# Performance work log

Measured on AMD Instinct MI355X. Metric: run time of the kernel, lower is better.

The kernel has to match this reference:

```python
import jax, jax.numpy as jnp
import numpy as np

BN_EPS = 1e-5

def setup_inputs() -> dict:
    key = jax.random.key(0)
    ks = jax.random.split(key, 5)
    B, C, H, W = 4, 64, 64, 64
    s = 1.0 / np.sqrt(C)
    return {
        "x": jax.random.normal(ks[0], (B, C, H, W), dtype=jnp.float32),
        "Wk": jax.random.normal(ks[1], (C, C), dtype=jnp.float32) * s,
        "Wq": jax.random.normal(ks[2], (C, C), dtype=jnp.float32) * s,
        "Wv": jax.random.normal(ks[3], (C, C), dtype=jnp.float32) * s,
        "W2": jax.random.normal(ks[4], (C, C), dtype=jnp.float32) * s,
        "gamma": jnp.ones((C,), dtype=jnp.float32),
        "beta": jnp.zeros((C,), dtype=jnp.float32),
        "running_mean": jnp.zeros((C,), dtype=jnp.float32),
        "running_var": jnp.ones((C,), dtype=jnp.float32),
    }

def reference(x, Wk, Wq, Wv, W2, gamma, beta, running_mean, running_var):
    B, C, H, W = x.shape
    N = H * W
    xf = x.reshape(B, C, N)                      # flatten spatial -> (B,C,N)
    # 1x1 convs (no bias) == channel matmuls
    k = jnp.einsum('oc,bcn->bon', Wk, xf)        # (B,C,N)
    q = jnp.einsum('oc,bcn->bon', Wq, xf)
    v = jnp.einsum('oc,bcn->bon', Wv, xf)
    # scores[b,n,m] = sum_c k[b,c,n] * q[b,c,m]  (note: no 1/sqrt(d) scaling, as in source)
    scores = jnp.einsum('bcn,bcm->bnm', k, q)    # (B,N,N)
    p = jax.nn.softmax(scores, axis=2)
    # att[b,c,n] = sum_m p[b,n,m] * v[b,c,m]
    att = jnp.einsum('bnm,bcm->bcn', p, v)       # (B,C,N)
    y = jnp.einsum('oc,bcn->bon', W2, att)       # 1x1 conv
    inv = gamma / jnp.sqrt(running_var + BN_EPS)
    y = y * inv[None, :, None] + (beta - running_mean * inv)[None, :, None]
    y = jax.nn.relu(y)
    return y.reshape(B, C, H, W) + x
```

## Files before the change

### kernel.cpp

```cpp
#include <hip/hip_runtime.h>

#define CH   64
#define NTOT 4096
#define NB   4
#define L2E  1.44269504088896340736f

typedef short  short4v  __attribute__((ext_vector_type(4)));
typedef short  short8v  __attribute__((ext_vector_type(8)));
typedef float  floatx4  __attribute__((ext_vector_type(4)));

static __device__ __forceinline__ unsigned pk2bf(float lo, float hi) {
    unsigned r;
    asm("v_cvt_pk_bf16_f32 %0, %1, %2" : "=v"(r) : "v"(lo), "v"(hi));
    return r;
}
static __device__ __forceinline__ float ex2(float x) {
    return __builtin_amdgcn_exp2f(x);
}
static __device__ __forceinline__ short f2bf(float f) {
    union { float f; unsigned u; } v; v.f = f;
    unsigned r = v.u + 0x7FFFu + ((v.u >> 16) & 1u);
    return (short)(r >> 16);
}
static __device__ __forceinline__ float bf2f(short s) {
    union { unsigned u; float f; } v; v.u = ((unsigned)(unsigned short)s) << 16;
    return v.f;
}

__global__ __launch_bounds__(256) void qkv_mfma(
    const float* __restrict__ x,
    const float* __restrict__ Wk, const float* __restrict__ Wq,
    const float* __restrict__ Wv,
    short* __restrict__ kT, short* __restrict__ qT, short* __restrict__ vg)
{
    __shared__ __align__(16) short xhi[64 * 72];
    __shared__ __align__(16) short xlo[64 * 72];
    __shared__ __align__(16) short whi[64 * 72];
    __shared__ __align__(16) short wlo[64 * 72];

    const int tid = threadIdx.x;
    const int w = tid >> 6, l = tid & 63, g = l >> 4, ln = l & 15;
    const int b  = blockIdx.x >> 6;
    const int n0 = (blockIdx.x & 63) << 6;
    const float* xb = x + ((size_t)b << 18);

    #pragma unroll
    for (int i = 0; i < 4; ++i) {
        int idx = tid + (i << 8);
        int c = idx >> 4, n4 = (idx & 15) << 2;
        float4 xv = *(const float4*)&xb[c * 4096 + n0 + n4];
        float xa[4] = {xv.x, xv.y, xv.z, xv.w};
        #pragma unroll
        for (int j = 0; j < 4; ++j) {
            short h = f2bf(xa[j]);
            xhi[(n4 + j) * 72 + c] = h;
            xlo[(n4 + j) * 72 + c] = f2bf(xa[j] - bf2f(h));
        }
    }

    const int wo = tid >> 2, wc = (tid & 3) << 4;
    #pragma unroll
    for (int j2 = 0; j2 < 4; ++j2) {
        float4 a = *(const float4*)&Wk[wo * 64 + wc + (j2 << 2)];
        float aa[4] = {a.x, a.y, a.z, a.w};
        #pragma unroll
        for (int j = 0; j < 4; ++j) {
            short h = f2bf(aa[j]);
            whi[wo * 72 + wc + (j2 << 2) + j] = h;
            wlo[wo * 72 + wc + (j2 << 2) + j] = f2bf(aa[j] - bf2f(h));
        }
    }
    __syncthreads();

    short8v xh0 = *(const short8v*)&xhi[((w << 4) + ln) * 72 + (g << 3)];
    short8v xh1 = *(const short8v*)&xhi[((w << 4) + ln) * 72 + 32 + (g << 3)];
    short8v xl0 = *(const short8v*)&xlo[((w << 4) + ln) * 72 + (g << 3)];
    short8v xl1 = *(const short8v*)&xlo[((w << 4) + ln) * 72 + 32 + (g << 3)];

    #pragma unroll
    for (int m = 0; m < 3; ++m) {
        if (m > 0) {
            const float* W = (m == 1) ? Wq : Wv;
            #pragma unroll
            for (int j2 = 0; j2 < 4; ++j2) {
                float4 a = *(const float4*)&W[wo * 64 + wc + (j2 << 2)];
                float aa[4] = {a.x, a.y, a.z, a.w};
                #pragma unroll
                for (int j = 0; j < 4; ++j) {
                    short h = f2bf(aa[j]);
                    whi[wo * 72 + wc + (j2 << 2) + j] = h;
                    wlo[wo * 72 + wc + (j2 << 2) + j] = f2bf(aa[j] - bf2f(h));
                }
            }
            __syncthreads();
        }

        #pragma unroll
        for (int ot = 0; ot < 4; ++ot) {
            short8v ah0 = *(const short8v*)&whi[((ot << 4) + ln) * 72 + (g << 3)];
            short8v ah1 = *(const short8v*)&whi[((ot << 4) + ln) * 72 + 32 + (g << 3)];
            short8v al0 = *(const short8v*)&wlo[((ot << 4) + ln) * 72 + (g << 3)];
            short8v al1 = *(const short8v*)&wlo[((ot << 4) + ln) * 72 + 32 + (g << 3)];
            floatx4 acc = (floatx4){0.f, 0.f, 0.f, 0.f};
            if (m < 2) {
                acc = __builtin_amdgcn_mfma_f32_16x16x32_bf16(ah0, xh0, acc, 0, 0, 0);
                acc = __builtin_amdgcn_mfma_f32_16x16x32_bf16(ah1, xh1, acc, 0, 0, 0);
                acc = __builtin_amdgcn_mfma_f32_16x16x32_bf16(al0, xh0, acc, 0, 0, 0);
                acc = __builtin_amdgcn_mfma_f32_16x16x32_bf16(al1, xh1, acc, 0, 0, 0);
                acc = __builtin_amdgcn_mfma_f32_16x16x32_bf16(ah0, xl0, acc, 0, 0, 0);
                acc = __builtin_amdgcn_mfma_f32_16x16x32_bf16(ah1, xl1, acc, 0, 0, 0);
                short* dst = ((m == 0) ? kT : qT) + ((size_t)b << 18);
                uint2 p;
                p.x = pk2bf(acc[0], acc[1]);
                p.y = pk2bf(acc[2], acc[3]);
                *(uint2*)&dst[(size_t)(n0 + (w << 4) + ln) * 64 + (ot << 4) + (g << 2)] = p;
            } else {
                acc = __builtin_amdgcn_mfma_f32_16x16x32_bf16(xh0, ah0, acc, 0, 0, 0);
                acc = __builtin_amdgcn_mfma_f32_16x16x32_bf16(xh1, ah1, acc, 0, 0, 0);
                acc = __builtin_amdgcn_mfma_f32_16x16x32_bf16(xl0, ah0, acc, 0, 0, 0);
                acc = __builtin_amdgcn_mfma_f32_16x16x32_bf16(xl1, ah1, acc, 0, 0, 0);
                acc = __builtin_amdgcn_mfma_f32_16x16x32_bf16(xh0, al0, acc, 0, 0, 0);
                acc = __builtin_amdgcn_mfma_f32_16x16x32_bf16(xh1, al1, acc, 0, 0, 0);
                short* dst = vg + ((size_t)b << 18);
                uint2 p;
                p.x = pk2bf(acc[0], acc[1]);
                p.y = pk2bf(acc[2], acc[3]);
                *(uint2*)&dst[(size_t)((ot << 4) + ln) * 4096 + n0 + (w << 4) + (g << 2)] = p;
            }
        }
        __syncthreads();
    }
}

__global__ __launch_bounds__(256) void attn_partial(
    const short* __restrict__ kT, const short* __restrict__ qT,
    const short* __restrict__ vg,
    float* __restrict__ opart, float* __restrict__ mlpart)
{
    __shared__ __align__(16) short smem[27648];

    const int tid = threadIdx.x;
    const int w = tid >> 6, l = tid & 63, g = l >> 4, ln = l & 15;

    const int bid = blockIdx.x;
    const int xcd = bid & 7, grp = bid >> 3;
    const int bk  = (xcd << 1) | (grp >> 5);
    const int b   = bk >> 2, kc = bk & 3;
    const int qblk = grp & 31;
    const int n0   = qblk << 7;
    const int part = (((b << 2) | kc) << 5) | qblk;
    const int kbase = kc << 10;

    const short* kTb = kT + ((size_t)b << 18) + (size_t)n0 * 64;
    const short* qTb = qT + ((size_t)b << 18);
    const short* vb  = vg + ((size_t)b << 18);

    short* const kTs = smem;
    short* const qS  = smem + 9216;
    short* const vS  = smem + 13824;
    short* const PsW = smem + 18432 + w * 2304;

    #pragma unroll
    for (int j = 0; j < 4; ++j) {
        int row = tid >> 1, c8 = ((tid & 1) << 5) + (j << 3);
        *(short8v*)&kTs[row * 72 + c8] = *(const short8v*)&kTb[row * 64 + c8];
    }
    __syncthreads();

    short8v bS0 = *(const short8v*)&kTs[((w << 5) + ln) * 72 + (g << 3)];
    short8v bS1 = *(const short8v*)&kTs[((w << 5) + ln) * 72 + 32 + (g << 3)];
    short8v bS2 = *(const short8v*)&kTs[((w << 5) + 16 + ln) * 72 + (g << 3)];
    short8v bS3 = *(const short8v*)&kTs[((w << 5) + 16 + ln) * 72 + 32 + (g << 3)];

    float mrun0 = -1e30f, lrun0 = 0.f;
    float mrun1 = -1e30f, lrun1 = 0.f;
    floatx4 acc0[4], acc1[4];
    #pragma unroll
    for (int ct = 0; ct < 4; ++ct) {
        acc0[ct] = (floatx4){0.f, 0.f, 0.f, 0.f};
        acc1[ct] = (floatx4){0.f, 0.f, 0.f, 0.f};
    }

    const int i0 = tid, i1 = tid + 256;

    short8v pf[4];
    pf[0] = *(const short8v*)&qTb[(size_t)(kbase + (i0 >> 3)) * 64 + ((i0 & 7) << 3)];
    pf[1] = *(const short8v*)&qTb[(size_t)(kbase + (i1 >> 3)) * 64 + ((i1 & 7) << 3)];
    pf[2] = *(const short8v*)&vb[(size_t)(i0 >> 3) * 4096 + kbase + ((i0 & 7) << 3)];
    pf[3] = *(const short8v*)&vb[(size_t)(i1 >> 3) * 4096 + kbase + ((i1 & 7) << 3)];

    for (int t = 0; t < 16; ++t) {
        __syncthreads();
        *(short8v*)&qS[(i0 >> 3) * 72 + ((i0 & 7) << 3)] = pf[0];
        *(short8v*)&qS[(i1 >> 3) * 72 + ((i1 & 7) << 3)] = pf[1];
        *(short8v*)&vS[(i0 >> 3) * 72 + ((i0 & 7) << 3)] = pf[2];
        *(short8v*)&vS[(i1 >> 3) * 72 + ((i1 & 7) << 3)] = pf[3];
        __syncthreads();
        if (t < 15) {
            int m1 = kbase + ((t + 1) << 6);
            pf[0] = *(const short8v*)&qTb[(size_t)(m1 + (i0 >> 3)) * 64 + ((i0 & 7) << 3)];
            pf[1] = *(const short8v*)&qTb[(size_t)(m1 + (i1 >> 3)) * 64 + ((i1 & 7) << 3)];
            pf[2] = *(const short8v*)&vb[(size_t)(i0 >> 3) * 4096 + m1 + ((i0 & 7) << 3)];
            pf[3] = *(const short8v*)&vb[(size_t)(i1 >> 3) * 4096 + m1 + ((i1 & 7) << 3)];
        }

        floatx4 s0[4], s1[4];
        #pragma unroll
        for (int mt = 0; mt < 4; ++mt) {
            short8v a0 = *(const short8v*)&qS[((mt << 4) + ln) * 72 + (g << 3)];
            short8v a1 = *(const short8v*)&qS[((mt << 4) + ln) * 72 + 32 + (g << 3)];
            floatx4 acc = (floatx4){0.f, 0.f, 0.f, 0.f};
            acc = __builtin_amdgcn_mfma_f32_16x16x32_bf16(a0, bS0, acc, 0, 0, 0);
            acc = __builtin_amdgcn_mfma_f32_16x16x32_bf16(a1, bS1, acc, 0, 0, 0);
            s0[mt] = acc;
            acc = (floatx4){0.f, 0.f, 0.f, 0.f};
            acc = __builtin_amdgcn_mfma_f32_16x16x32_bf16(a0, bS2, acc, 0, 0, 0);
            acc = __builtin_amdgcn_mfma_f32_16x16x32_bf16(a1, bS3, acc, 0, 0, 0);
            s1[mt] = acc;
        }

        {
            float mx = s0[0][0];
            #pragma unroll
            for (int mt = 0; mt < 4; ++mt)
                #pragma unroll
                for (int r = 0; r < 4; ++r) mx = fmaxf(mx, s0[mt][r]);
            mx = fmaxf(mx, __shfl_xor(mx, 16));
            mx = fmaxf(mx, __shfl_xor(mx, 32));
            if (!__all(mx <= mrun0)) {
                float mnew = fmaxf(mrun0, mx);
                float fs = ex2((mrun0 - mnew) * L2E);
                mrun0 = mnew;
                lrun0 *= fs;
                #pragma unroll
                for (int ct = 0; ct < 4; ++ct) {
                    acc0[ct][0] *= fs; acc0[ct][1] *= fs;
                    acc0[ct][2] *= fs; acc0[ct][3] *= fs;
                }
            }
            const float nm = -mrun0 * L2E;
            float s = 0.f;
            #pragma unroll
            for (int mt = 0; mt < 4; ++mt) {
                float p0 = ex2(__builtin_fmaf(s0[mt][0], L2E, nm));
                float p1 = ex2(__builtin_fmaf(s0[mt][1], L2E, nm));
                float p2 = ex2(__builtin_fmaf(s0[mt][2], L2E, nm));
                float p3 = ex2(__builtin_fmaf(s0[mt][3], L2E, nm));
                s += (p0 + p1) + (p2 + p3);
                uint2 pkv;
                pkv.x = pk2bf(p0, p1);
                pkv.y = pk2bf(p2, p3);
                *(uint2*)&PsW[ln * 72 + (mt << 4) + (g << 2)] = pkv;
            }
            s += __shfl_xor(s, 16);
            s += __shfl_xor(s, 32);
            lrun0 += s;
        }
        {
            float mx = s1[0][0];
            #pragma unroll
            for (int mt = 0; mt < 4; ++mt)
                #pragma unroll
                for (int r = 0; r < 4; ++r) mx = fmaxf(mx, s1[mt][r]);
            mx = fmaxf(mx, __shfl_xor(mx, 16));
            mx = fmaxf(mx, __shfl_xor(mx, 32));
            if (!__all(mx <= mrun1)) {
                float mnew = fmaxf(mrun1, mx);
                float fs = ex2((mrun1 - mnew) * L2E);
                mrun1 = mnew;
                lrun1 *= fs;
                #pragma unroll
                for (int ct = 0; ct < 4; ++ct) {
                    acc1[ct][0] *= fs; acc1[ct][1] *= fs;
                    acc1[ct][2] *= fs; acc1[ct][3] *= fs;
                }
            }
            const float nm = -mrun1 * L2E;
            float s = 0.f;
            #pragma unroll
            for (int mt = 0; mt < 4; ++mt) {
                float p0 = ex2(__builtin_fmaf(s1[mt][0], L2E, nm));
                float p1 = ex2(__builtin_fmaf(s1[mt][1], L2E, nm));
                float p2 = ex2(__builtin_fmaf(s1[mt][2], L2E, nm));
                float p3 = ex2(__builtin_fmaf(s1[mt][3], L2E, nm));
                s += (p0 + p1) + (p2 + p3);
                uint2 pkv;
                pkv.x = pk2bf(p0, p1);
                pkv.y = pk2bf(p2, p3);
                *(uint2*)&PsW[(16 + ln) * 72 + (mt << 4) + (g << 2)] = pkv;
            }
            s += __shfl_xor(s, 16);
            s += __shfl_xor(s, 32);
            lrun1 += s;
        }

        short8v bp0 = *(const short8v*)&PsW[ln * 72 + (g << 3)];
        short8v bp1 = *(const short8v*)&PsW[ln * 72 + 32 + (g << 3)];
        short8v bp2 = *(const short8v*)&PsW[(16 + ln) * 72 + (g << 3)];
        short8v bp3 = *(const short8v*)&PsW[(16 + ln) * 72 + 32 + (g << 3)];
        #pragma unroll
        for (int ct = 0; ct < 4; ++ct) {
            short8v a0 = *(const short8v*)&vS[((ct << 4) + ln) * 72 + (g << 3)];
            short8v a1 = *(const short8v*)&vS[((ct << 4) + ln) * 72 + 32 + (g << 3)];
            acc0[ct] = __builtin_amdgcn_mfma_f32_16x16x32_bf16(a0, bp0, acc0[ct], 0, 0, 0);
            acc0[ct] = __builtin_amdgcn_mfma_f32_16x16x32_bf16(a1, bp1, acc0[ct], 0, 0, 0);
            acc1[ct] = __builtin_amdgcn_mfma_f32_16x16x32_bf16(a0, bp2, acc1[ct], 0, 0, 0);
            acc1[ct] = __builtin_amdgcn_mfma_f32_16x16x32_bf16(a1, bp3, acc1[ct], 0, 0, 0);
        }
    }

    __syncthreads();
    float* xp = (float*)(smem + 9216);
    #pragma unroll
    for (int ct = 0; ct < 4; ++ct)
        #pragma unroll
        for (int r = 0; r < 4; ++r) {
            xp[((w << 5) + ln) * 68 + (ct << 4) + (g << 2) + r]      = acc0[ct][r];
            xp[((w << 5) + 16 + ln) * 68 + (ct << 4) + (g << 2) + r] = acc1[ct][r];
        }
    if (g == 0) {
        mlpart[(size_t)part * 256 + (w << 5) + ln]            = mrun0;
        mlpart[(size_t)part * 256 + (w << 5) + 16 + ln]       = mrun1;
        mlpart[(size_t)part * 256 + 128 + (w << 5) + ln]      = lrun0;
        mlpart[(size_t)part * 256 + 128 + (w << 5) + 16 + ln] = lrun1;
    }
    __syncthreads();
    {
        int q = tid >> 1, c32 = (tid & 1) << 5;
        float* Ob = opart + (size_t)part * 8192 + q * 64 + c32;
        const float* Xp = &xp[q * 68 + c32];
        #pragma unroll
        for (int j = 0; j < 8; ++j)
            *(float4*)&Ob[j << 2] = *(const float4*)&Xp[j << 2];
    }
}

__global__ __launch_bounds__(256) void attn_merge(
    const float* __restrict__ opart, const float* __restrict__ mlpart,
    const float* __restrict__ W2,
    const float* __restrict__ gamma, const float* __restrict__ beta,
    const float* __restrict__ rmean, const float* __restrict__ rvar,
    const float* __restrict__ x, float* __restrict__ out)
{
    __shared__ __align__(16) short attL[64 * 72];
    __shared__ __align__(16) short w2s [64 * 72];
    __shared__ float wgt[4][64];
    __shared__ float linv[64];

    const int tid = threadIdx.x;
    const int w = tid >> 6, l = tid & 63, g = l >> 4, ln = l & 15;

    const int b      = blockIdx.x >> 6;
    const int qblk64 = blockIdx.x & 63;
    const int n0     = qblk64 << 6;
    const int qb128  = qblk64 >> 1;
    const int qoff   = (qblk64 & 1) << 6;

    if (tid < 64) {
        float mv[4], lv[4];
        #pragma unroll
        for (int kc = 0; kc < 4; ++kc) {
            int part = (((b << 2) | kc) << 5) | qb128;
            mv[kc] = mlpart[(size_t)part * 256 + qoff + tid];
            lv[kc] = mlpart[(size_t)part * 256 + 128 + qoff + tid];
        }
        float mm = fmaxf(fmaxf(mv[0], mv[1]), fmaxf(mv[2], mv[3]));
        float den = 0.f;
        #pragma unroll
        for (int kc = 0; kc < 4; ++kc) {
            float wk = ex2((mv[kc] - mm) * L2E);
            wgt[kc][tid] = wk;
            den += wk * lv[kc];
        }
        linv[tid] = 1.0f / den;
    }
    for (int i = tid; i < 1024; i += 256) {
        int r = i >> 4, c4 = (i & 15) << 2;
        float4 wv = *(const float4*)&W2[(r << 6) + c4];
        uint2 s4;
        s4.x = pk2bf(wv.x, wv.y);
        s4.y = pk2bf(wv.z, wv.w);
        *(uint2*)&w2s[r * 72 + c4] = s4;
    }
    __syncthreads();

    {
        int q = tid >> 2, c16 = (tid & 3) << 4;
        float a[16] = {};
        #pragma unroll
        for (int kc = 0; kc < 4; ++kc) {
            int part = (((b << 2) | kc) << 5) | qb128;
            float wk = wgt[kc][q];
            const float* Ob = opart + (size_t)part * 8192 + (qoff + q) * 64 + c16;
            #pragma unroll
            for (int i = 0; i < 4; ++i) {
                float4 o4 = *(const float4*)&Ob[i << 2];
                a[(i << 2) + 0] += wk * o4.x;
                a[(i << 2) + 1] += wk * o4.y;
                a[(i << 2) + 2] += wk * o4.z;
                a[(i << 2) + 3] += wk * o4.w;
            }
        }
        float li = linv[q];
        #pragma unroll
        for (int i = 0; i < 4; ++i) {
            uint2 s4;
            s4.x = pk2bf(a[(i << 2) + 0] * li, a[(i << 2) + 1] * li);
            s4.y = pk2bf(a[(i << 2) + 2] * li, a[(i << 2) + 3] * li);
            *(uint2*)&attL[q * 72 + c16 + (i << 2)] = s4;
        }
    }
    __syncthreads();

    short8v bA0 = *(const short8v*)&attL[((w << 4) + ln) * 72 + (g << 3)];
    short8v bA1 = *(const short8v*)&attL[((w << 4) + ln) * 72 + 32 + (g << 3)];
    const int nq = n0 + (w << 4) + ln;
    #pragma unroll
    for (int ot = 0; ot < 4; ++ot) {
        short8v a0 = *(const short8v*)&w2s[((ot << 4) + ln) * 72 + (g << 3)];
        short8v a1 = *(const short8v*)&w2s[((ot << 4) + ln) * 72 + 32 + (g << 3)];
        floatx4 acc = (floatx4){0.f, 0.f, 0.f, 0.f};
        acc = __builtin_amdgcn_mfma_f32_16x16x32_bf16(a0, bA0, acc, 0, 0, 0);
        acc = __builtin_amdgcn_mfma_f32_16x16x32_bf16(a1, bA1, acc, 0, 0, 0);
        int o0 = (ot << 4) + (g << 2);
        float4 gm = *(const float4*)&gamma[o0];
        float4 bt = *(const float4*)&beta [o0];
        float4 rm = *(const float4*)&rmean[o0];
        float4 rv = *(const float4*)&rvar [o0];
        float gma[4] = {gm.x, gm.y, gm.z, gm.w};
        float bta[4] = {bt.x, bt.y, bt.z, bt.w};
        float rma[4] = {rm.x, rm.y, rm.z, rm.w};
        float rva[4] = {rv.x, rv.y, rv.z, rv.w};
        #pragma unroll
        for (int r = 0; r < 4; ++r) {
            float inv  = gma[r] * __frsqrt_rn(rva[r] + 1e-5f);
            float bias = bta[r] - rma[r] * inv;
            size_t ga = (((size_t)(b << 6) + o0 + r) << 12) + nq;
            out[ga] = fmaxf(acc[r] * inv + bias, 0.f) + x[ga];
        }
    }
}

extern "C" void kernel_launch(void* const* d_in, const int* in_sizes, int n_in,
                              void* d_out, int out_size, void* d_ws, size_t ws_size,
                              hipStream_t stream)
{
    const float* x     = (const float*)d_in[0];
    const float* Wk    = (const float*)d_in[1];
    const float* Wq    = (const float*)d_in[2];
    const float* Wv    = (const float*)d_in[3];
    const float* W2    = (const float*)d_in[4];
    const float* gamma = (const float*)d_in[5];
    const float* beta  = (const float*)d_in[6];
    const float* rmean = (const float*)d_in[7];
    const float* rvar  = (const float*)d_in[8];
    float* out = (float*)d_out;

    const size_t plane = (size_t)NB * NTOT * CH;
    short* kT = (short*)d_ws;
    short* qT = kT + plane;
    short* vv = qT + plane;
    float* opart  = (float*)(vv + plane);
    float* mlpart = opart + (size_t)512 * 8192;

    qkv_mfma    <<<dim3(256), dim3(256), 0, stream>>>(x, Wk, Wq, Wv, kT, qT, vv);
    attn_partial<<<dim3(512), dim3(256), 0, stream>>>(kT, qT, vv, opart, mlpart);
    attn_merge  <<<dim3(256), dim3(256), 0, stream>>>(opart, mlpart, W2, gamma, beta,
                                                      rmean, rvar, x, out);
}
```

Before: 62.88 us.

## Load attention Q/V fragments straight from global, drop LDS staging and block barriers

The attention partial kernel no longer stages K, Q and V tiles through shared memory with block-wide barriers. Each wave now loads its MFMA operands directly from global memory in 32-key steps and keeps only a per-wave LDS region for the probability tile and the output transpose. MFMA sections are wrapped in s_setprio so matrix work gets issue priority. This removes __syncthreads and LDS traffic and cuts LDS use, which may raise occupancy. In exchange, every wave re-reads the same Q/V data from global/L2, the V loads are strided, and there is no explicit prefetch, so load latency may be exposed.

```diff
diff --git a/kernel.cpp b/kernel.cpp
--- a/kernel.cpp
+++ b/kernel.cpp
@@ -26,6 +26,8 @@
     union { unsigned u; float f; } v; v.u = ((unsigned)(unsigned short)s) << 16;
     return v.f;
 }
+
+#define MFMA16(A, B, C) __builtin_amdgcn_mfma_f32_16x16x32_bf16(A, B, C, 0, 0, 0)
 
 __global__ __launch_bounds__(256) void qkv_mfma(
     const float* __restrict__ x,
@@ -103,24 +105,24 @@
             short8v al1 = *(const short8v*)&wlo[((ot << 4) + ln) * 72 + 32 + (g << 3)];
             floatx4 acc = (floatx4){0.f, 0.f, 0.f, 0.f};
             if (m < 2) {
-                acc = __builtin_amdgcn_mfma_f32_16x16x32_bf16(ah0, xh0, acc, 0, 0, 0);
-                acc = __builtin_amdgcn_mfma_f32_16x16x32_bf16(ah1, xh1, acc, 0, 0, 0);
-                acc = __builtin_amdgcn_mfma_f32_16x16x32_bf16(al0, xh0, acc, 0, 0, 0);
-                acc = __builtin_amdgcn_mfma_f32_16x16x32_bf16(al1, xh1, acc, 0, 0, 0);
-                acc = __builtin_amdgcn_mfma_f32_16x16x32_bf16(ah0, xl0, acc, 0, 0, 0);
-                acc = __builtin_amdgcn_mfma_f32_16x16x32_bf16(ah1, xl1, acc, 0, 0, 0);
+                acc = MFMA16(ah0, xh0, acc);
+                acc = MFMA16(ah1, xh1, acc);
+                acc = MFMA16(al0, xh0, acc);
+                acc = MFMA16(al1, xh1, acc);
+                acc = MFMA16(ah0, xl0, acc);
+                acc = MFMA16(ah1, xl1, acc);
                 short* dst = ((m == 0) ? kT : qT) + ((size_t)b << 18);
                 uint2 p;
                 p.x = pk2bf(acc[0], acc[1]);
                 p.y = pk2bf(acc[2], acc[3]);
                 *(uint2*)&dst[(size_t)(n0 + (w << 4) + ln) * 64 + (ot << 4) + (g << 2)] = p;
             } else {
-                acc = __builtin_amdgcn_mfma_f32_16x16x32_bf16(xh0, ah0, acc, 0, 0, 0);
-                acc = __builtin_amdgcn_mfma_f32_16x16x32_bf16(xh1, ah1, acc, 0, 0, 0);
-                acc = __builtin_amdgcn_mfma_f32_16x16x32_bf16(xl0, ah0, acc, 0, 0, 0);
-                acc = __builtin_amdgcn_mfma_f32_16x16x32_bf16(xl1, ah1, acc, 0, 0, 0);
-                acc = __builtin_amdgcn_mfma_f32_16x16x32_bf16(xh0, al0, acc, 0, 0, 0);
-                acc = __builtin_amdgcn_mfma_f32_16x16x32_bf16(xh1, al1, acc, 0, 0, 0);
+                acc = MFMA16(xh0, ah0, acc);
+                acc = MFMA16(xh1, ah1, acc);
+                acc = MFMA16(xl0, ah0, acc);
+                acc = MFMA16(xl1, ah1, acc);
+                acc = MFMA16(xh0, al0, acc);
+                acc = MFMA16(xh1, al1, acc);
                 short* dst = vg + ((size_t)b << 18);
                 uint2 p;
                 p.x = pk2bf(acc[0], acc[1]);
@@ -137,7 +139,7 @@
     const short* __restrict__ vg,
     float* __restrict__ opart, float* __restrict__ mlpart)
 {
-    __shared__ __align__(16) short smem[27648];
+    __shared__ __align__(16) short smem[4 * 4352];
 
     const int tid = threadIdx.x;
     const int w = tid >> 6, l = tid & 63, g = l >> 4, ln = l & 15;
@@ -151,26 +153,19 @@
     const int part = (((b << 2) | kc) << 5) | qblk;
     const int kbase = kc << 10;
 
-    const short* kTb = kT + ((size_t)b << 18) + (size_t)n0 * 64;
+    const short* kTb = kT + ((size_t)b << 18);
     const short* qTb = qT + ((size_t)b << 18);
     const short* vb  = vg + ((size_t)b << 18);
 
-    short* const kTs = smem;
-    short* const qS  = smem + 9216;
-    short* const vS  = smem + 13824;
-    short* const PsW = smem + 18432 + w * 2304;
-
-    #pragma unroll
-    for (int j = 0; j < 4; ++j) {
-        int row = tid >> 1, c8 = ((tid & 1) << 5) + (j << 3);
-        *(short8v*)&kTs[row * 72 + c8] = *(const short8v*)&kTb[row * 64 + c8];
-    }
-    __syncthreads();
-
-    short8v bS0 = *(const short8v*)&kTs[((w << 5) + ln) * 72 + (g << 3)];
-    short8v bS1 = *(const short8v*)&kTs[((w << 5) + ln) * 72 + 32 + (g << 3)];
-    short8v bS2 = *(const short8v*)&kTs[((w << 5) + 16 + ln) * 72 + (g << 3)];
-    short8v bS3 = *(const short8v*)&kTs[((w << 5) + 16 + ln) * 72 + 32 + (g << 3)];
+    short* const PsW = smem + w * 4352;
+    float* const xp  = (float*)(smem + w * 4352);
+
+    const size_t qr0 = (size_t)(n0 + (w << 5) + ln) * 64;
+    const size_t qr1 = (size_t)(n0 + (w << 5) + 16 + ln) * 64;
+    short8v bS0 = *(const short8v*)&kTb[qr0 + (g << 3)];
+    short8v bS1 = *(const short8v*)&kTb[qr0 + 32 + (g << 3)];
+    short8v bS2 = *(const short8v*)&kTb[qr1 + (g << 3)];
+    short8v bS3 = *(const short8v*)&kTb[qr1 + 32 + (g << 3)];
 
     float mrun0 = -1e30f, lrun0 = 0.f;
     float mrun1 = -1e30f, lrun1 = 0.f;
@@ -181,50 +176,30 @@
         acc1[ct] = (floatx4){0.f, 0.f, 0.f, 0.f};
     }
 
-    const int i0 = tid, i1 = tid + 256;
-
-    short8v pf[4];
-    pf[0] = *(const short8v*)&qTb[(size_t)(kbase + (i0 >> 3)) * 64 + ((i0 & 7) << 3)];
-    pf[1] = *(const short8v*)&qTb[(size_t)(kbase + (i1 >> 3)) * 64 + ((i1 & 7) << 3)];
-    pf[2] = *(const short8v*)&vb[(size_t)(i0 >> 3) * 4096 + kbase + ((i0 & 7) << 3)];
-    pf[3] = *(const short8v*)&vb[(size_t)(i1 >> 3) * 4096 + kbase + ((i1 & 7) << 3)];
-
-    for (int t = 0; t < 16; ++t) {
-        __syncthreads();
-        *(short8v*)&qS[(i0 >> 3) * 72 + ((i0 & 7) << 3)] = pf[0];
-        *(short8v*)&qS[(i1 >> 3) * 72 + ((i1 & 7) << 3)] = pf[1];
-        *(short8v*)&vS[(i0 >> 3) * 72 + ((i0 & 7) << 3)] = pf[2];
-        *(short8v*)&vS[(i1 >> 3) * 72 + ((i1 & 7) << 3)] = pf[3];
-        __syncthreads();
-        if (t < 15) {
-            int m1 = kbase + ((t + 1) << 6);
-            pf[0] = *(const short8v*)&qTb[(size_t)(m1 + (i0 >> 3)) * 64 + ((i0 & 7) << 3)];
-            pf[1] = *(const short8v*)&qTb[(size_t)(m1 + (i1 >> 3)) * 64 + ((i1 & 7) << 3)];
-            pf[2] = *(const short8v*)&vb[(size_t)(i0 >> 3) * 4096 + m1 + ((i0 & 7) << 3)];
-            pf[3] = *(const short8v*)&vb[(size_t)(i1 >> 3) * 4096 + m1 + ((i1 & 7) << 3)];
-        }
-
-        floatx4 s0[4], s1[4];
-        #pragma unroll
-        for (int mt = 0; mt < 4; ++mt) {
-            short8v a0 = *(const short8v*)&qS[((mt << 4) + ln) * 72 + (g << 3)];
-            short8v a1 = *(const short8v*)&qS[((mt << 4) + ln) * 72 + 32 + (g << 3)];
-            floatx4 acc = (floatx4){0.f, 0.f, 0.f, 0.f};
-            acc = __builtin_amdgcn_mfma_f32_16x16x32_bf16(a0, bS0, acc, 0, 0, 0);
-            acc = __builtin_amdgcn_mfma_f32_16x16x32_bf16(a1, bS1, acc, 0, 0, 0);
-            s0[mt] = acc;
-            acc = (floatx4){0.f, 0.f, 0.f, 0.f};
-            acc = __builtin_amdgcn_mfma_f32_16x16x32_bf16(a0, bS2, acc, 0, 0, 0);
-            acc = __builtin_amdgcn_mfma_f32_16x16x32_bf16(a1, bS3, acc, 0, 0, 0);
-            s1[mt] = acc;
-        }
+    for (int t = 0; t < 32; ++t) {
+        const int m0 = kbase + (t << 5);
+
+        short8v ka00 = *(const short8v*)&qTb[(size_t)(m0 + ln) * 64 + (g << 3)];
+        short8v ka01 = *(const short8v*)&qTb[(size_t)(m0 + ln) * 64 + 32 + (g << 3)];
+        short8v ka10 = *(const short8v*)&qTb[(size_t)(m0 + 16 + ln) * 64 + (g << 3)];
+        short8v ka11 = *(const short8v*)&qTb[(size_t)(m0 + 16 + ln) * 64 + 32 + (g << 3)];
+        short8v va0 = *(const short8v*)&vb[(size_t)(ln)      * 4096 + m0 + (g << 3)];
+        short8v va1 = *(const short8v*)&vb[(size_t)(16 + ln) * 4096 + m0 + (g << 3)];
+        short8v va2 = *(const short8v*)&vb[(size_t)(32 + ln) * 4096 + m0 + (g << 3)];
+        short8v va3 = *(const short8v*)&vb[(size_t)(48 + ln) * 4096 + m0 + (g << 3)];
+
+        floatx4 s00, s01, s10, s11;
+        floatx4 z = (floatx4){0.f, 0.f, 0.f, 0.f};
+        __builtin_amdgcn_s_setprio(1);
+        s00 = MFMA16(ka00, bS0, z);  s00 = MFMA16(ka01, bS1, s00);
+        s01 = MFMA16(ka10, bS0, z);  s01 = MFMA16(ka11, bS1, s01);
+        s10 = MFMA16(ka00, bS2, z);  s10 = MFMA16(ka01, bS3, s10);
+        s11 = MFMA16(ka10, bS2, z);  s11 = MFMA16(ka11, bS3, s11);
+        __builtin_amdgcn_s_setprio(0);
 
         {
-            float mx = s0[0][0];
-            #pragma unroll
-            for (int mt = 0; mt < 4; ++mt)
-                #pragma unroll
-                for (int r = 0; r < 4; ++r) mx = fmaxf(mx, s0[mt][r]);
+            float mx = fmaxf(fmaxf(fmaxf(s00[0], s00[1]), fmaxf(s00[2], s00[3])),
+                             fmaxf(fmaxf(s01[0], s01[1]), fmaxf(s01[2], s01[3])));
             mx = fmaxf(mx, __shfl_xor(mx, 16));
             mx = fmaxf(mx, __shfl_xor(mx, 32));
             if (!__all(mx <= mrun0)) {
@@ -239,29 +214,27 @@
                 }
             }
             const float nm = -mrun0 * L2E;
-            float s = 0.f;
-            #pragma unroll
-            for (int mt = 0; mt < 4; ++mt) {
-                float p0 = ex2(__builtin_fmaf(s0[mt][0], L2E, nm));
-                float p1 = ex2(__builtin_fmaf(s0[mt][1], L2E, nm));
-                float p2 = ex2(__builtin_fmaf(s0[mt][2], L2E, nm));
-                float p3 = ex2(__builtin_fmaf(s0[mt][3], L2E, nm));
-                s += (p0 + p1) + (p2 + p3);
-                uint2 pkv;
-                pkv.x = pk2bf(p0, p1);
-                pkv.y = pk2bf(p2, p3);
-                *(uint2*)&PsW[ln * 72 + (mt << 4) + (g << 2)] = pkv;
-            }
+            float p0 = ex2(__builtin_fmaf(s00[0], L2E, nm));
+            float p1 = ex2(__builtin_fmaf(s00[1], L2E, nm));
+            float p2 = ex2(__builtin_fmaf(s00[2], L2E, nm));
+            float p3 = ex2(__builtin_fmaf(s00[3], L2E, nm));
+            float p4 = ex2(__builtin_fmaf(s01[0], L2E, nm));
+            float p5 = ex2(__builtin_fmaf(s01[1], L2E, nm));
+            float p6 = ex2(__builtin_fmaf(s01[2], L2E, nm));
+            float p7 = ex2(__builtin_fmaf(s01[3], L2E, nm));
+            uint2 pa, pb;
+            pa.x = pk2bf(p0, p1);  pa.y = pk2bf(p2, p3);
+            pb.x = pk2bf(p4, p5);  pb.y = pk2bf(p6, p7);
+            *(uint2*)&PsW[ln * 40 + (g << 2)]      = pa;
+            *(uint2*)&PsW[ln * 40 + 16 + (g << 2)] = pb;
+            float s = ((p0 + p1) + (p2 + p3)) + ((p4 + p5) + (p6 + p7));
             s += __shfl_xor(s, 16);
             s += __shfl_xor(s, 32);
             lrun0 += s;
         }
         {
-            float mx = s1[0][0];
-            #pragma unroll
-            for (int mt = 0; mt < 4; ++mt)
-                #pragma unroll
-                for (int r = 0; r < 4; ++r) mx = fmaxf(mx, s1[mt][r]);
+            float mx = fmaxf(fmaxf(fmaxf(s10[0], s10[1]), fmaxf(s10[2], s10[3])),
+                             fmaxf(fmaxf(s11[0], s11[1]), fmaxf(s11[2], s11[3])));
             mx = fmaxf(mx, __shfl_xor(mx, 16));
             mx = fmaxf(mx, __shfl_xor(mx, 32));
             if (!__all(mx <= mrun1)) {
@@ -276,47 +249,41 @@
                 }
             }
             const float nm = -mrun1 * L2E;
-            float s = 0.f;
-            #pragma unroll
-            for (int mt = 0; mt < 4; ++mt) {
-                float p0 = ex2(__builtin_fmaf(s1[mt][0], L2E, nm));
-                float p1 = ex2(__builtin_fmaf(s1[mt][1], L2E, nm));
-                float p2 = ex2(__builtin_fmaf(s1[mt][2], L2E, nm));
-                float p3 = ex2(__builtin_fmaf(s1[mt][3], L2E, nm));
-                s += (p0 + p1) + (p2 + p3);
-                uint2 pkv;
-                pkv.x = pk2bf(p0, p1);
-                pkv.y = pk2bf(p2, p3);
-                *(uint2*)&PsW[(16 + ln) * 72 + (mt << 4) + (g << 2)] = pkv;
-            }
+            float p0 = ex2(__builtin_fmaf(s10[0], L2E, nm));
+            float p1 = ex2(__builtin_fmaf(s10[1], L2E, nm));
+            float p2 = ex2(__builtin_fmaf(s10[2], L2E, nm));
+            float p3 = ex2(__builtin_fmaf(s10[3], L2E, nm));
+            float p4 = ex2(__builtin_fmaf(s11[0], L2E, nm));
+            float p5 = ex2(__builtin_fmaf(s11[1], L2E, nm));
+            float p6 = ex2(__builtin_fmaf(s11[2], L2E, nm));
+            float p7 = ex2(__builtin_fmaf(s11[3], L2E, nm));
+            uint2 pa, pb;
+            pa.x = pk2bf(p0, p1);  pa.y = pk2bf(p2, p3);
+            pb.x = pk2bf(p4, p5);  pb.y = pk2bf(p6, p7);
+            *(uint2*)&PsW[(16 + ln) * 40 + (g << 2)]      = pa;
+            *(uint2*)&PsW[(16 + ln) * 40 + 16 + (g << 2)] = pb;
+            float s = ((p0 + p1) + (p2 + p3)) + ((p4 + p5) + (p6 + p7));
             s += __shfl_xor(s, 16);
             s += __shfl_xor(s, 32);
             lrun1 += s;
         }
 
-        short8v bp0 = *(const short8v*)&PsW[ln * 72 + (g << 3)];
-        short8v bp1 = *(const short8v*)&PsW[ln * 72 + 32 + (g << 3)];
-        short8v bp2 = *(const short8v*)&PsW[(16 + ln) * 72 + (g << 3)];
-        short8v bp3 = *(const short8v*)&PsW[(16 + ln) * 72 + 32 + (g << 3)];
-        #pragma unroll
-        for (int ct = 0; ct < 4; ++ct) {
-            short8v a0 = *(const short8v*)&vS[((ct << 4) + ln) * 72 + (g << 3)];
-            short8v a1 = *(const short8v*)&vS[((ct << 4) + ln) * 72 + 32 + (g << 3)];
-            acc0[ct] = __builtin_amdgcn_mfma_f32_16x16x32_bf16(a0, bp0, acc0[ct], 0, 0, 0);
-            acc0[ct] = __builtin_amdgcn_mfma_f32_16x16x32_bf16(a1, bp1, acc0[ct], 0, 0, 0);
-            acc1[ct] = __builtin_amdgcn_mfma_f32_16x16x32_bf16(a0, bp2, acc1[ct], 0, 0, 0);
-            acc1[ct] = __builtin_amdgcn_mfma_f32_16x16x32_bf16(a1, bp3, acc1[ct], 0, 0, 0);
-        }
-    }
-
-    __syncthreads();
-    float* xp = (float*)(smem + 9216);
+        short8v bp0 = *(const short8v*)&PsW[ln * 40 + (g << 3)];
+        short8v bp1 = *(const short8v*)&PsW[(16 + ln) * 40 + (g << 3)];
+        __builtin_amdgcn_s_setprio(1);
+        acc0[0] = MFMA16(va0, bp0, acc0[0]);  acc1[0] = MFMA16(va0, bp1, acc1[0]);
+        acc0[1] = MFMA16(va1, bp0, acc0[1]);  acc1[1] = MFMA16(va1, bp1, acc1[1]);
+        acc0[2] = MFMA16(va2, bp0, acc0[2]);  acc1[2] = MFMA16(va2, bp1, acc1[2]);
+        acc0[3] = MFMA16(va3, bp0, acc0[3]);  acc1[3] = MFMA16(va3, bp1, acc1[3]);
+        __builtin_amdgcn_s_setprio(0);
+    }
+
     #pragma unroll
     for (int ct = 0; ct < 4; ++ct)
         #pragma unroll
         for (int r = 0; r < 4; ++r) {
-            xp[((w << 5) + ln) * 68 + (ct << 4) + (g << 2) + r]      = acc0[ct][r];
-            xp[((w << 5) + 16 + ln) * 68 + (ct << 4) + (g << 2) + r] = acc1[ct][r];
+            xp[ln * 68 + (ct << 4) + (g << 2) + r]        = acc0[ct][r];
+            xp[(16 + ln) * 68 + (ct << 4) + (g << 2) + r] = acc1[ct][r];
         }
     if (g == 0) {
         mlpart[(size_t)part * 256 + (w << 5) + ln]            = mrun0;
@@ -324,11 +291,10 @@
         mlpart[(size_t)part * 256 + 128 + (w << 5) + ln]      = lrun0;
         mlpart[(size_t)part * 256 + 128 + (w << 5) + 16 + ln] = lrun1;
     }
-    __syncthreads();
     {
-        int q = tid >> 1, c32 = (tid & 1) << 5;
-        float* Ob = opart + (size_t)part * 8192 + q * 64 + c32;
-        const float* Xp = &xp[q * 68 + c32];
+        int lq = l >> 1, c0 = (l & 1) << 5;
+        float* Ob = opart + (size_t)part * 8192 + (size_t)((w << 5) + lq) * 64 + c0;
+        const float* Xp = &xp[lq * 68 + c0];
         #pragma unroll
         for (int j = 0; j < 8; ++j)
             *(float4*)&Ob[j << 2] = *(const float4*)&Xp[j << 2];
@@ -420,8 +386,8 @@
         short8v a0 = *(const short8v*)&w2s[((ot << 4) + ln) * 72 + (g << 3)];
         short8v a1 = *(const short8v*)&w2s[((ot << 4) + ln) * 72 + 32 + (g << 3)];
         floatx4 acc = (floatx4){0.f, 0.f, 0.f, 0.f};
-        acc = __builtin_amdgcn_mfma_f32_16x16x32_bf16(a0, bA0, acc, 0, 0, 0);
-        acc = __builtin_amdgcn_mfma_f32_16x16x32_bf16(a1, bA1, acc, 0, 0, 0);
+        acc = MFMA16(a0, bA0, acc);
+        acc = MFMA16(a1, bA1, acc);
         int o0 = (ot << 4) + (g << 2);
         float4 gm = *(const float4*)&gamma[o0];
         float4 bt = *(const float4*)&beta [o0];
```

Result: slower. 89.29 us (+42.0%).
